# Optimization experiments

Measured on AMD Instinct MI355X. Metric: run time of the kernel, lower is better.

## Reference

```python
import jax, jax.numpy as jnp
import numpy as np

# Model dims
B, S, D = 1, 768, 256          # batch, seq_len, d_model
H, KD = 8, 256                 # num_heads, key_dim
DH = KD // H                   # head_dim = 32
BS, NR, W, G = 64, 3, 3, 1     # block_size, num_rand_blocks, window_size, global_tokens
NEG = -1e9


def _build_sparse_indices(seed=0):
    """Replicates _create_sparse_attention_mask (sparse branch) with numpy.
    Returns (attn_indices [S, M] int32 clamped >=0, blocked_mask [1,1,S,M] float32)."""
    nb = S // BS  # num_blocks (S divisible by BS here)
    rng = np.random.RandomState(seed)
    r = np.arange(nb)
    # window pairs |i - j| <= W
    ii, jj = np.meshgrid(r, r, indexing='ij')
    win = np.abs(ii - jj) <= W
    window_pairs = np.stack([ii[win], jj[win]], axis=1)
    # global: every block -> first G blocks; first G blocks -> every block
    g = np.arange(G)
    glob_to = np.stack([np.repeat(r, G), np.tile(g, nb)], axis=1)
    glob_from = np.stack([np.repeat(g, nb), np.tile(r, G)], axis=1)
    # random pairs
    rand_pairs = rng.randint(0, nb, size=(NR * nb, 2))
    allp = np.concatenate([window_pairs, glob_to, glob_from, rand_pairs], axis=0)
    uniq = np.unique(allp[:, 0] * nb + allp[:, 1])  # sorted unique (row, col)
    rows, cols = uniq // nb, uniq % nb
    max_row = int(np.max(np.bincount(rows, minlength=nb)))
    M = max_row * BS  # padded neighbor-token width (= S when a global block is dense)
    idx = np.full((nb, M), -1, dtype=np.int64)
    for b in range(nb):
        cs = cols[rows == b]
        toks = (cs[:, None] * BS + np.arange(BS)[None, :]).reshape(-1)
        idx[b, :toks.size] = toks
    tok_idx = idx[np.arange(S) // BS]  # expand per-block rows to per-token rows [S, M]
    mask = np.where(tok_idx >= 0, 0.0, NEG).astype(np.float32)
    return np.maximum(tok_idx, 0).astype(np.int32), mask[None, None]


def setup_inputs() -> dict:
    key = jax.random.key(0)
    ks = jax.random.split(key, 8)

    def dense_w(k, fi, fo):  # glorot-uniform like keras Dense
        lim = float(np.sqrt(6.0 / (fi + fo)))
        return jax.random.uniform(k, (fi, fo), jnp.float32, -lim, lim)

    attn_indices, blocked_mask = _build_sparse_indices()
    return {
        'query': jax.random.normal(ks[0], (B, S, D), jnp.float32),
        'value': jax.random.normal(ks[1], (B, S, D), jnp.float32),
        'key_in': jax.random.normal(ks[2], (B, S, D), jnp.float32),
        'Wq': dense_w(ks[3], D, KD), 'bq': jnp.zeros((KD,), jnp.float32),
        'Wk': dense_w(ks[4], D, KD), 'bk': jnp.zeros((KD,), jnp.float32),
        'Wv': dense_w(ks[5], D, KD), 'bv': jnp.zeros((KD,), jnp.float32),
        'Wo': dense_w(ks[6], KD, D), 'bo': jnp.zeros((D,), jnp.float32),
        'attn_indices': jnp.asarray(attn_indices),
        'blocked_mask': jnp.asarray(blocked_mask),
    }


def reference(query, value, key_in, Wq, bq, Wk, bk, Wv, bv, Wo, bo, attn_indices, blocked_mask):
    q = query @ Wq + bq
    k = key_in @ Wk + bk
    v = value @ Wv + bv

    def split_heads(x):  # [B,S,KD] -> [B*H,S,DH]
        return x.reshape(B, S, H, DH).transpose(0, 2, 1, 3).reshape(B * H, S, DH)

    q = split_heads(q) * (DH ** -0.5)
    k = split_heads(k)
    v = split_heads(v)

    # gather sparse neighbor tokens (indices shared across batch*heads)
    k_g = jnp.take(k, attn_indices, axis=1)  # [BH, S, M, DH]
    v_g = jnp.take(v, attn_indices, axis=1)  # [BH, S, M, DH]

    scores = jnp.einsum('bnd,bnmd->bnm', q, k_g)  # [BH, S, M]
    M = attn_indices.shape[1]
    scores = scores.reshape(B, H, S, M) + blocked_mask  # pad positions -> -1e9
    probs = jax.nn.softmax(scores, axis=-1)

    ctx = jnp.einsum('bnm,bnmd->bnd', probs.reshape(B * H, S, M), v_g)  # [BH,S,DH]
    ctx = ctx.reshape(B, H, S, DH).transpose(0, 2, 1, 3).reshape(B, S, KD)
    out = ctx @ Wo + bo
    return out, scores, attn_indices
```

## Files before the change

kernel.cpp:

```cpp
#include <hip/hip_runtime.h>
#include <math.h>

#define SQ 768
#define DMODEL 256
#define NH 8
#define DHD 32
#define NB 12
#define QSCALE 0.1767766952966369f
#define PSHIFT 8.0f

__global__ __launch_bounds__(256) void proj3(
    const float* __restrict__ query, const float* __restrict__ value,
    const float* __restrict__ key_in,
    const float* __restrict__ Wq, const float* __restrict__ bq,
    const float* __restrict__ Wk, const float* __restrict__ bk,
    const float* __restrict__ Wv, const float* __restrict__ bv,
    const float* __restrict__ bo, float* __restrict__ outbuf,
    const int* __restrict__ aidx, float* __restrict__ idx_out,
    float* __restrict__ qhp, float* __restrict__ khp, float* __restrict__ vhp)
{
    const int j = threadIdx.x;

    {
        const int bidf = blockIdx.y * 96 + blockIdx.x;
        const int i0 = (bidf * 256 + j) * 8;
        int4 a = *(const int4*)&aidx[i0];
        int4 b = *(const int4*)&aidx[i0 + 4];
        *(float4*)&idx_out[i0] =
            make_float4((float)a.x, (float)a.y, (float)a.z, (float)a.w);
        *(float4*)&idx_out[i0 + 4] =
            make_float4((float)b.x, (float)b.y, (float)b.z, (float)b.w);
    }

    const int s0 = blockIdx.x * 8;
    const int w  = blockIdx.y;

    if (w == 0) {
        const float bb = bo[j];
        #pragma unroll
        for (int r = 0; r < 8; ++r)
            outbuf[(s0 + r) * DMODEL + j] = bb;
    }

    const float *X, *W, *bias; float* outp; float scale;
    if (w == 0)      { X = query;  W = Wq; bias = bq; outp = qhp; scale = QSCALE; }
    else if (w == 1) { X = key_in; W = Wk; bias = bk; outp = khp; scale = 1.0f; }
    else             { X = value;  W = Wv; bias = bv; outp = vhp; scale = 1.0f; }

    __shared__ __align__(16) float xs[8][DMODEL];
    {
        float* xsf = &xs[0][0];
        const float* Xp = X + s0 * DMODEL;
        const int i0 = j * 8;
        *(float4*)&xsf[i0]     = *(const float4*)&Xp[i0];
        *(float4*)&xsf[i0 + 4] = *(const float4*)&Xp[i0 + 4];
    }
    __syncthreads();

    const int j0 = (j & 127) * 2;
    const int r0 = (j >> 7) * 4;

    float acc[4][2] = {};
    #pragma unroll 2
    for (int k4 = 0; k4 < DMODEL / 4; ++k4) {
        float4 x0 = *(const float4*)&xs[r0 + 0][k4 * 4];
        float4 x1 = *(const float4*)&xs[r0 + 1][k4 * 4];
        float4 x2 = *(const float4*)&xs[r0 + 2][k4 * 4];
        float4 x3 = *(const float4*)&xs[r0 + 3][k4 * 4];
        const float xr[4][4] = {
            {x0.x, x0.y, x0.z, x0.w}, {x1.x, x1.y, x1.z, x1.w},
            {x2.x, x2.y, x2.z, x2.w}, {x3.x, x3.y, x3.z, x3.w}};
        #pragma unroll
        for (int kk = 0; kk < 4; ++kk) {
            const float2 wv = *(const float2*)&W[(k4 * 4 + kk) * DMODEL + j0];
            #pragma unroll
            for (int i = 0; i < 4; ++i) {
                acc[i][0] = fmaf(xr[i][kk], wv.x, acc[i][0]);
                acc[i][1] = fmaf(xr[i][kk], wv.y, acc[i][1]);
            }
        }
    }

    const float2 bb = *(const float2*)&bias[j0];
    const int h = j0 >> 5, d = j0 & 31;
    #pragma unroll
    for (int i = 0; i < 4; ++i) {
        float2 o;
        o.x = (acc[i][0] + bb.x) * scale;
        o.y = (acc[i][1] + bb.y) * scale;
        *(float2*)&outp[h * (SQ * DHD) + (s0 + r0 + i) * DHD + d] = o;
    }
}

__global__ __launch_bounds__(512) void attn2(
    const float* __restrict__ qh, const float* __restrict__ kh,
    const float* __restrict__ vh, const int* __restrict__ aidx,
    const float* __restrict__ mask, const float* __restrict__ Wo,
    float* __restrict__ scores_out, float* __restrict__ out, int M)
{
    __shared__ __align__(16) float Ks[2][2][32][68];
    __shared__ __align__(16) float Vs[2][2][64][36];
    __shared__ __align__(16) float Ps[2][32][68];
    __shared__ float dot0s[32];
    __shared__ float invL[32];

    const int b    = blockIdx.x;
    const int half = blockIdx.y;
    const int h    = blockIdx.z;
    const int s0b  = b * 64;
    const int s0   = s0b + half * 32;
    const int tid  = threadIdx.x;
    const int u    = tid >> 8;
    const int utid = tid & 255;
    const int NCH2 = M / 128;

    const int qrt = (utid & 15) * 2;
    const int qct = (utid >> 4) * 4;
    const int rp  = utid & 15;
    const int dg  = (utid >> 4) & 3;
    const int cg  = utid >> 6;
    const int c   = utid & 63;
    const int sg  = utid >> 6;
    const int d4a = sg * 4;
    const int d4b = 16 + sg * 4;

    const float* mrow = &mask[s0b * M];
    const int*   arow = &aidx[s0b * M];
    float*       srow = &scores_out[(h * SQ + s0) * M];

    float qr0[32], qr1[32];
    {
        const float* qp = &qh[(h * SQ + s0 + qrt) * DHD];
        #pragma unroll
        for (int d4 = 0; d4 < DHD; d4 += 4) {
            float4 a  = *(const float4*)&qp[d4];
            float4 b4 = *(const float4*)&qp[DHD + d4];
            qr0[d4] = a.x;  qr0[d4+1] = a.y;  qr0[d4+2] = a.z;  qr0[d4+3] = a.w;
            qr1[d4] = b4.x; qr1[d4+1] = b4.y; qr1[d4+2] = b4.z; qr1[d4+3] = b4.w;
        }
    }

    if (tid < 16) {
        const float* k0 = &kh[h * SQ * DHD];
        float a0 = 0.f, a1 = 0.f;
        #pragma unroll
        for (int d = 0; d < DHD; ++d) {
            const float kv = k0[d];
            a0 = fmaf(qr0[d], kv, a0);
            a1 = fmaf(qr1[d], kv, a1);
        }
        dot0s[qrt] = a0; dot0s[qrt + 1] = a1;
    }

    float mv_cur = mrow[(u * NCH2) * 64];
    bool  val_cur = mv_cur > -0.5f;
    if (val_cur) {
        const int t0 = arow[(u * NCH2) * 64];
        const float* kp = &kh[(h * SQ + t0 + c) * DHD];
        const float* vp = &vh[(h * SQ + t0 + c) * DHD];
        float4 ka = *(const float4*)&kp[d4a];
        float4 kb = *(const float4*)&kp[d4b];
        Ks[u][0][d4a+0][c] = ka.x; Ks[u][0][d4a+1][c] = ka.y;
        Ks[u][0][d4a+2][c] = ka.z; Ks[u][0][d4a+3][c] = ka.w;
        Ks[u][0][d4b+0][c] = kb.x; Ks[u][0][d4b+1][c] = kb.y;
        Ks[u][0][d4b+2][c] = kb.z; Ks[u][0][d4b+3][c] = kb.w;
        *(float4*)&Vs[u][0][c][d4a] = *(const float4*)&vp[d4a];
        *(float4*)&Vs[u][0][c][d4b] = *(const float4*)&vp[d4b];
    }
    __syncthreads();

    float4 acc0a = make_float4(0.f,0.f,0.f,0.f), acc0b = acc0a;
    float4 acc1a = acc0a, acc1b = acc0a;
    float rps0 = 0.f, rps1 = 0.f;
    int cur = 0;

    for (int ci = 0; ci < NCH2; ++ci) {
        const int m0 = (u * NCH2 + ci) * 64;

        bool  val_nxt = false;
        float mv_nxt  = 0.f;
        float4 ka, kb, va, vb;
        if (ci + 1 < NCH2) {
            mv_nxt  = mrow[m0 + 64];
            val_nxt = mv_nxt > -0.5f;
            if (val_nxt) {
                const int t0 = arow[m0 + 64];
                const float* kp = &kh[(h * SQ + t0 + c) * DHD];
                const float* vp = &vh[(h * SQ + t0 + c) * DHD];
                ka = *(const float4*)&kp[d4a];
                kb = *(const float4*)&kp[d4b];
                va = *(const float4*)&vp[d4a];
                vb = *(const float4*)&vp[d4b];
            }
        }

        if (val_cur) {
            const float* Kb = &Ks[u][cur][0][qct];
            float sc[2][4] = {};
            #pragma unroll
            for (int kk = 0; kk < 32; ++kk) {
                float4 b4 = *(const float4*)&Kb[kk * 68];
                sc[0][0] = fmaf(qr0[kk], b4.x, sc[0][0]);
                sc[0][1] = fmaf(qr0[kk], b4.y, sc[0][1]);
                sc[0][2] = fmaf(qr0[kk], b4.z, sc[0][2]);
                sc[0][3] = fmaf(qr0[kk], b4.w, sc[0][3]);
                sc[1][0] = fmaf(qr1[kk], b4.x, sc[1][0]);
                sc[1][1] = fmaf(qr1[kk], b4.y, sc[1][1]);
                sc[1][2] = fmaf(qr1[kk], b4.z, sc[1][2]);
                sc[1][3] = fmaf(qr1[kk], b4.w, sc[1][3]);
            }
            {
                *(float4*)&srow[(qrt + 0) * M + m0 + qct] =
                    make_float4(sc[0][0], sc[0][1], sc[0][2], sc[0][3]);
                float4 e;
                e.x = __expf(sc[0][0] - PSHIFT); e.y = __expf(sc[0][1] - PSHIFT);
                e.z = __expf(sc[0][2] - PSHIFT); e.w = __expf(sc[0][3] - PSHIFT);
                *(float4*)&Ps[u][qrt + 0][qct] = e;
                rps0 += (e.x + e.y) + (e.z + e.w);
            }
            {
                *(float4*)&srow[(qrt + 1) * M + m0 + qct] =
                    make_float4(sc[1][0], sc[1][1], sc[1][2], sc[1][3]);
                float4 e;
                e.x = __expf(sc[1][0] - PSHIFT); e.y = __expf(sc[1][1] - PSHIFT);
                e.z = __expf(sc[1][2] - PSHIFT); e.w = __expf(sc[1][3] - PSHIFT);
                *(float4*)&Ps[u][qrt + 1][qct] = e;
                rps1 += (e.x + e.y) + (e.z + e.w);
            }
        } else {
            #pragma unroll
            for (int i = 0; i < 8; ++i) {
                const int e = utid + i * 256;
                const int r = e >> 6, cc = e & 63;
                srow[r * M + m0 + cc] = dot0s[r] + mv_cur;
            }
        }

        if (val_nxt) {
            Ks[u][cur^1][d4a+0][c] = ka.x; Ks[u][cur^1][d4a+1][c] = ka.y;
            Ks[u][cur^1][d4a+2][c] = ka.z; Ks[u][cur^1][d4a+3][c] = ka.w;
            Ks[u][cur^1][d4b+0][c] = kb.x; Ks[u][cur^1][d4b+1][c] = kb.y;
            Ks[u][cur^1][d4b+2][c] = kb.z; Ks[u][cur^1][d4b+3][c] = kb.w;
            *(float4*)&Vs[u][cur^1][c][d4a] = va;
            *(float4*)&Vs[u][cur^1][c][d4b] = vb;
        }
        __syncthreads();

        if (val_cur) {
            const float (*Vb)[36] = Vs[u][cur];
            const float* Pr0 = &Ps[u][2 * rp][0];
            const float* Pr1 = &Ps[u][2 * rp + 1][0];
            const int c0 = cg * 16;
            const int dd = dg * 8;
            #pragma unroll
            for (int k = 0; k < 4; ++k) {
                float4 pa = *(const float4*)&Pr0[c0 + k * 4];
                float4 pb = *(const float4*)&Pr1[c0 + k * 4];
                const float pav[4] = {pa.x, pa.y, pa.z, pa.w};
                const float pbv[4] = {pb.x, pb.y, pb.z, pb.w};
                #pragma unroll
                for (int t = 0; t < 4; ++t) {
                    const int cc2 = c0 + k * 4 + t;
                    float4 v0 = *(const float4*)&Vb[cc2][dd];
                    float4 v1 = *(const float4*)&Vb[cc2][dd + 4];
                    acc0a.x = fmaf(pav[t], v0.x, acc0a.x);
                    acc0a.y = fmaf(pav[t], v0.y, acc0a.y);
                    acc0a.z = fmaf(pav[t], v0.z, acc0a.z);
                    acc0a.w = fmaf(pav[t], v0.w, acc0a.w);
                    acc0b.x = fmaf(pav[t], v1.x, acc0b.x);
                    acc0b.y = fmaf(pav[t], v1.y, acc0b.y);
                    acc0b.z = fmaf(pav[t], v1.z, acc0b.z);
                    acc0b.w = fmaf(pav[t], v1.w, acc0b.w);
                    acc1a.x = fmaf(pbv[t], v0.x, acc1a.x);
                    acc1a.y = fmaf(pbv[t], v0.y, acc1a.y);
                    acc1a.z = fmaf(pbv[t], v0.z, acc1a.z);
                    acc1a.w = fmaf(pbv[t], v0.w, acc1a.w);
                    acc1b.x = fmaf(pbv[t], v1.x, acc1b.x);
                    acc1b.y = fmaf(pbv[t], v1.y, acc1b.y);
                    acc1b.z = fmaf(pbv[t], v1.z, acc1b.z);
                    acc1b.w = fmaf(pbv[t], v1.w, acc1b.w);
                }
            }
        }
        __syncthreads();

        val_cur = val_nxt; mv_cur = mv_nxt; cur ^= 1;
    }

    float* vacc = &Vs[0][0][0][0];
    float* rsum = &Ps[0][0][0];
    {
        const int s = u * 4 + cg;
        float* base = vacc + (s * 32 + 2 * rp) * 36 + dg * 8;
        *(float4*)&base[0]  = acc0a; *(float4*)&base[4]  = acc0b;
        *(float4*)&base[36] = acc1a; *(float4*)&base[40] = acc1b;
        const int qg = utid >> 4;
        rsum[(u * 16 + qg) * 32 + qrt]     = rps0;
        rsum[(u * 16 + qg) * 32 + qrt + 1] = rps1;
    }
    __syncthreads();

    if (tid < 32) {
        float pt = 0.f;
        #pragma unroll
        for (int s2 = 0; s2 < 32; ++s2) pt += rsum[s2 * 32 + tid];
        invL[tid] = 1.0f / pt;
    }
    __syncthreads();

    float* ctxn = &Ks[0][0][0][0];
    if (tid < 256) {
        const int r = tid & 31, dq = tid >> 5;
        float4 sum = make_float4(0.f, 0.f, 0.f, 0.f);
        #pragma unroll
        for (int s = 0; s < 8; ++s) {
            float4 v = *(const float4*)&vacc[(s * 32 + r) * 36 + dq * 4];
            sum.x += v.x; sum.y += v.y; sum.z += v.z; sum.w += v.w;
        }
        const float il = invL[r];
        sum.x *= il; sum.y *= il; sum.z *= il; sum.w *= il;
        *(float4*)&ctxn[r * 36 + dq * 4] = sum;
    }
    __syncthreads();

    {
        const int jc = tid & 255, rg = tid >> 8;
        float wo[32];
        #pragma unroll
        for (int k = 0; k < 32; ++k)
            wo[k] = Wo[(h * DHD + k) * DMODEL + jc];
        for (int rr = rg * 16; rr < rg * 16 + 16; ++rr) {
            float a = 0.f;
            #pragma unroll
            for (int k4 = 0; k4 < 8; ++k4) {
                float4 cv = *(const float4*)&ctxn[rr * 36 + k4 * 4];
                a = fmaf(cv.x, wo[k4 * 4 + 0], a);
                a = fmaf(cv.y, wo[k4 * 4 + 1], a);
                a = fmaf(cv.z, wo[k4 * 4 + 2], a);
                a = fmaf(cv.w, wo[k4 * 4 + 3], a);
            }
            atomicAdd(&out[(s0 + rr) * DMODEL + jc], a);
        }
    }
}

extern "C" void kernel_launch(void* const* d_in, const int* in_sizes, int n_in,
                              void* d_out, int out_size, void* d_ws, size_t ws_size,
                              hipStream_t stream)
{
    const float* query  = (const float*)d_in[0];
    const float* value  = (const float*)d_in[1];
    const float* key_in = (const float*)d_in[2];
    const float* Wq = (const float*)d_in[3];
    const float* bq = (const float*)d_in[4];
    const float* Wk = (const float*)d_in[5];
    const float* bk = (const float*)d_in[6];
    const float* Wv = (const float*)d_in[7];
    const float* bv = (const float*)d_in[8];
    const float* Wo = (const float*)d_in[9];
    const float* bo = (const float*)d_in[10];
    const int*   aidx = (const int*)d_in[11];
    const float* mask = (const float*)d_in[12];

    const int M = in_sizes[11] / SQ;

    float* out        = (float*)d_out;
    float* scores_out = out + SQ * DMODEL;
    float* idx_out    = scores_out + NH * SQ * M;

    float* ws  = (float*)d_ws;
    float* qhp = ws;
    float* khp = qhp + NH * SQ * DHD;
    float* vhp = khp + NH * SQ * DHD;

    proj3<<<dim3(96, 3), 256, 0, stream>>>(
        query, value, key_in, Wq, bq, Wk, bk, Wv, bv,
        bo, out, aidx, idx_out, qhp, khp, vhp);

    attn2<<<dim3(NB, 2, NH), 512, 0, stream>>>(
        qhp, khp, vhp, aidx, mask, Wo, scores_out, out, M);
}
```

Measured before the change: 51.97 us.

## Double-buffer weight tiles in shared memory for QKV projection kernel

The QKV projection now stages 32-row chunks of the weight matrix into a double-buffered shared-memory tile, prefetching the next chunk into registers while computing the current one. Each thread computes a 2x4 output tile with float4 loads and stores instead of a 4x2 tile with direct global weight reads. This aims to cut the global-memory latency of W loads and raise arithmetic per load. It costs about 64 KB of extra LDS per block, which may reduce occupancy, and adds a barrier per chunk.

```diff
diff --git a/kernel.cpp b/kernel.cpp
--- a/kernel.cpp
+++ b/kernel.cpp
@@ -48,47 +48,86 @@
     else             { X = value;  W = Wv; bias = bv; outp = vhp; scale = 1.0f; }
 
     __shared__ __align__(16) float xs[8][DMODEL];
+    __shared__ __align__(16) float ws[2][32 * DMODEL];
+
     {
         float* xsf = &xs[0][0];
         const float* Xp = X + s0 * DMODEL;
         const int i0 = j * 8;
         *(float4*)&xsf[i0]     = *(const float4*)&Xp[i0];
         *(float4*)&xsf[i0 + 4] = *(const float4*)&Xp[i0 + 4];
+
+        #pragma unroll
+        for (int t = 0; t < 8; ++t)
+            *(float4*)&ws[0][t * 1024 + j * 4] =
+                *(const float4*)&W[t * 1024 + j * 4];
     }
     __syncthreads();
 
-    const int j0 = (j & 127) * 2;
-    const int r0 = (j >> 7) * 4;
-
-    float acc[4][2] = {};
-    #pragma unroll 2
-    for (int k4 = 0; k4 < DMODEL / 4; ++k4) {
-        float4 x0 = *(const float4*)&xs[r0 + 0][k4 * 4];
-        float4 x1 = *(const float4*)&xs[r0 + 1][k4 * 4];
-        float4 x2 = *(const float4*)&xs[r0 + 2][k4 * 4];
-        float4 x3 = *(const float4*)&xs[r0 + 3][k4 * 4];
-        const float xr[4][4] = {
-            {x0.x, x0.y, x0.z, x0.w}, {x1.x, x1.y, x1.z, x1.w},
-            {x2.x, x2.y, x2.z, x2.w}, {x3.x, x3.y, x3.z, x3.w}};
-        #pragma unroll
-        for (int kk = 0; kk < 4; ++kk) {
-            const float2 wv = *(const float2*)&W[(k4 * 4 + kk) * DMODEL + j0];
-            #pragma unroll
-            for (int i = 0; i < 4; ++i) {
-                acc[i][0] = fmaf(xr[i][kk], wv.x, acc[i][0]);
-                acc[i][1] = fmaf(xr[i][kk], wv.y, acc[i][1]);
-            }
-        }
-    }
-
-    const float2 bb = *(const float2*)&bias[j0];
+    const int j0 = (j & 63) * 4;
+    const int r0 = (j >> 6) * 2;
+
+    float4 acc0 = make_float4(0.f, 0.f, 0.f, 0.f);
+    float4 acc1 = make_float4(0.f, 0.f, 0.f, 0.f);
+    int cur = 0;
+
+    for (int c = 0; c < 8; ++c) {
+        float4 wreg[8];
+        if (c < 7) {
+            const float* Wc = W + (c + 1) * 8192;
+            #pragma unroll
+            for (int t = 0; t < 8; ++t)
+                wreg[t] = *(const float4*)&Wc[t * 1024 + j * 4];
+        }
+
+        const float* wb = &ws[cur][0];
+        #pragma unroll
+        for (int k4 = 0; k4 < 8; ++k4) {
+            const int kb = c * 32 + k4 * 4;
+            float4 x0 = *(const float4*)&xs[r0 + 0][kb];
+            float4 x1 = *(const float4*)&xs[r0 + 1][kb];
+            float4 w0 = *(const float4*)&wb[(k4 * 4 + 0) * DMODEL + j0];
+            float4 w1 = *(const float4*)&wb[(k4 * 4 + 1) * DMODEL + j0];
+            float4 w2 = *(const float4*)&wb[(k4 * 4 + 2) * DMODEL + j0];
+            float4 w3 = *(const float4*)&wb[(k4 * 4 + 3) * DMODEL + j0];
+            acc0.x = fmaf(x0.x, w0.x, acc0.x); acc0.y = fmaf(x0.x, w0.y, acc0.y);
+            acc0.z = fmaf(x0.x, w0.z, acc0.z); acc0.w = fmaf(x0.x, w0.w, acc0.w);
+            acc0.x = fmaf(x0.y, w1.x, acc0.x); acc0.y = fmaf(x0.y, w1.y, acc0.y);
+            acc0.z = fmaf(x0.y, w1.z, acc0.z); acc0.w = fmaf(x0.y, w1.w, acc0.w);
+            acc0.x = fmaf(x0.z, w2.x, acc0.x); acc0.y = fmaf(x0.z, w2.y, acc0.y);
+            acc0.z = fmaf(x0.z, w2.z, acc0.z); acc0.w = fmaf(x0.z, w2.w, acc0.w);
+            acc0.x = fmaf(x0.w, w3.x, acc0.x); acc0.y = fmaf(x0.w, w3.y, acc0.y);
+            acc0.z = fmaf(x0.w, w3.z, acc0.z); acc0.w = fmaf(x0.w, w3.w, acc0.w);
+            acc1.x = fmaf(x1.x, w0.x, acc1.x); acc1.y = fmaf(x1.x, w0.y, acc1.y);
+            acc1.z = fmaf(x1.x, w0.z, acc1.z); acc1.w = fmaf(x1.x, w0.w, acc1.w);
+            acc1.x = fmaf(x1.y, w1.x, acc1.x); acc1.y = fmaf(x1.y, w1.y, acc1.y);
+            acc1.z = fmaf(x1.y, w1.z, acc1.z); acc1.w = fmaf(x1.y, w1.w, acc1.w);
+            acc1.x = fmaf(x1.z, w2.x, acc1.x); acc1.y = fmaf(x1.z, w2.y, acc1.y);
+            acc1.z = fmaf(x1.z, w2.z, acc1.z); acc1.w = fmaf(x1.z, w2.w, acc1.w);
+            acc1.x = fmaf(x1.w, w3.x, acc1.x); acc1.y = fmaf(x1.w, w3.y, acc1.y);
+            acc1.z = fmaf(x1.w, w3.z, acc1.z); acc1.w = fmaf(x1.w, w3.w, acc1.w);
+        }
+
+        if (c < 7) {
+            float* wd = &ws[cur ^ 1][0];
+            #pragma unroll
+            for (int t = 0; t < 8; ++t)
+                *(float4*)&wd[t * 1024 + j * 4] = wreg[t];
+            __syncthreads();
+            cur ^= 1;
+        }
+    }
+
+    const float4 bb = *(const float4*)&bias[j0];
     const int h = j0 >> 5, d = j0 & 31;
-    #pragma unroll
-    for (int i = 0; i < 4; ++i) {
-        float2 o;
-        o.x = (acc[i][0] + bb.x) * scale;
-        o.y = (acc[i][1] + bb.y) * scale;
-        *(float2*)&outp[h * (SQ * DHD) + (s0 + r0 + i) * DHD + d] = o;
+    {
+        float4 o0, o1;
+        o0.x = (acc0.x + bb.x) * scale; o0.y = (acc0.y + bb.y) * scale;
+        o0.z = (acc0.z + bb.z) * scale; o0.w = (acc0.w + bb.w) * scale;
+        o1.x = (acc1.x + bb.x) * scale; o1.y = (acc1.y + bb.y) * scale;
+        o1.z = (acc1.z + bb.z) * scale; o1.w = (acc1.w + bb.w) * scale;
+        *(float4*)&outp[h * (SQ * DHD) + (s0 + r0 + 0) * DHD + d] = o0;
+        *(float4*)&outp[h * (SQ * DHD) + (s0 + r0 + 1) * DHD + d] = o1;
     }
 }
 
```

Result: faster. 48.88 us (median of 2 runs) (-5.9%).
